# Optimization experiments

Measured on AMD Instinct MI355X. Metric: run time of the kernel, lower is better.

The kernel has to match this reference:

```python
import jax, jax.numpy as jnp
import numpy as np
from functools import partial

DELTA_B = 30.0
DELTA_H = 30.0
NB = 12  # 360/30
NH = 12
E, H, A, MLP, T = 16, 32, 32, 128, 20


def setup_inputs() -> dict:
    key = jax.random.key(0)
    ks = jax.random.split(key, 32)
    B, N = 512, 32
    inp = {}
    inp['x'] = jax.random.normal(ks[0], (B, N, T, 2), jnp.float32)
    inp['dmat'] = jax.random.uniform(ks[1], (B, N, T, N), jnp.float32) * 10.0
    inp['bmat'] = jax.random.uniform(ks[2], (B, N, T, N), jnp.float32) * 360.0
    inp['hmat'] = jax.random.uniform(ks[3], (B, N, T, N), jnp.float32) * 360.0
    inp['mask'] = jnp.ones((B, N, T), jnp.float32)
    g = lambda k, sh, s=0.1: jax.random.normal(k, sh, jnp.float32) * s
    inp['emb_w'] = g(ks[4], (2, E)); inp['emb_b'] = jnp.zeros((E,), jnp.float32)
    inp['w_ih'] = g(ks[5], (E, 4 * H)); inp['w_hh'] = g(ks[6], (H, 4 * H))
    inp['b_ih'] = jnp.zeros((4 * H,), jnp.float32); inp['b_hh'] = jnp.zeros((4 * H,), jnp.float32)
    inp['enc2att_w'] = g(ks[7], (H, A)); inp['enc2att_b'] = jnp.zeros((A,), jnp.float32)
    inp['domain_tab'] = jnp.full((NB, NH), 5.0, jnp.float32)  # domain_parameter init
    inp['spemb_w'] = g(ks[8], (2 * A, A)); inp['spemb_b'] = jnp.zeros((A,), jnp.float32)
    inp['att2enc_w'] = g(ks[9], (A, H)); inp['att2enc_b'] = jnp.zeros((H,), jnp.float32)
    inp['cls_w1'] = g(ks[10], (T * H, MLP)); inp['cls_b1'] = jnp.zeros((MLP,), jnp.float32)
    inp['cls_w2'] = g(ks[11], (MLP, MLP)); inp['cls_b2'] = jnp.zeros((MLP,), jnp.float32)
    inp['cls_w3'] = g(ks[12], (MLP, 1)); inp['cls_b3'] = jnp.zeros((1,), jnp.float32)
    return inp


def _forward(x, dmat, bmat, hmat, mask, emb_w, emb_b, w_ih, w_hh, b_ih, b_hh,
             enc2att_w, enc2att_b, domain_tab, spemb_w, spemb_b,
             att2enc_w, att2enc_b, cls_w1, cls_b1, cls_w2, cls_b2, cls_w3, cls_b3):
    B, N = x.shape[0], x.shape[1]
    xe = x @ emb_w + emb_b                      # [B,N,T,E]
    # time-major sequences for scan
    seq = (jnp.moveaxis(xe, 2, 0), jnp.moveaxis(dmat, 2, 0), jnp.moveaxis(bmat, 2, 0),
           jnp.moveaxis(hmat, 2, 0), jnp.moveaxis(mask, 2, 0))
    h0 = jnp.zeros((B, N, H), xe.dtype)
    c0 = jnp.zeros((B, N, H), xe.dtype)

    def step(carry, inp):
        h, c = carry
        x_t, d_t, b_t, hd_t, m_t = inp
        gates = x_t @ w_ih + h @ w_hh + (b_ih + b_hh)   # [B,N,4H]
        i, f, g, o = jnp.split(gates, 4, axis=-1)
        c_new = jax.nn.sigmoid(f) * c + jax.nn.sigmoid(i) * jnp.tanh(g)
        h_lstm = jax.nn.sigmoid(o) * jnp.tanh(c_new)
        ha = h_lstm @ enc2att_w + enc2att_b              # enc2att -> [B,N,A]
        # spatial attention: domain value from bearing/heading bins vs distance
        ib = jnp.clip(jnp.floor(b_t / DELTA_B), 0, NB - 1).astype(jnp.int32)
        ih = jnp.clip(jnp.floor(hd_t / DELTA_H), 0, NH - 1).astype(jnp.int32)
        w = jax.nn.relu(domain_tab[ib, ih] - d_t)        # [B,N,N]
        w = w * m_t[:, :, None] * m_t[:, None, :]
        w = w / (w.sum(-1, keepdims=True) + 1e-8)
        att = jnp.einsum('bij,bjd->bid', w, ha)          # neighbor-weighted hidden
        emb = jnp.tanh(jnp.concatenate([ha, att], -1) @ spemb_w + spemb_b)
        h_new = emb @ att2enc_w + att2enc_b              # back to hidden_size
        return (h_new, c_new), h_new

    (_, _), hs = jax.lax.scan(step, (h0, c0), seq)       # hs: [T,B,N,H]
    enc = jnp.moveaxis(hs, 0, 2).reshape(B, N, T * H)
    z = jax.nn.leaky_relu(enc @ cls_w1 + cls_b1, 0.2)
    z = jax.nn.leaky_relu(z @ cls_w2 + cls_b2, 0.2)
    return jax.nn.sigmoid(z @ cls_w3 + cls_b3)           # [B,N,1]


def reference(x, dmat, bmat, hmat, mask, emb_w, emb_b, w_ih, w_hh, b_ih, b_hh,
              enc2att_w, enc2att_b, domain_tab, spemb_w, spemb_b,
              att2enc_w, att2enc_b, cls_w1, cls_b1, cls_w2, cls_b2, cls_w3, cls_b3):
    return _forward(x, dmat, bmat, hmat, mask, emb_w, emb_b, w_ih, w_hh, b_ih, b_hh,
                    enc2att_w, enc2att_b, domain_tab, spemb_w, spemb_b,
                    att2enc_w, att2enc_b, cls_w1, cls_b1, cls_w2, cls_b2, cls_w3, cls_b3)
```

## Files before the change

### kernel.cpp

```cpp
#include <hip/hip_runtime.h>
#include <hip/hip_bf16.h>

#define TD_B 512

typedef __bf16 bf16x8 __attribute__((ext_vector_type(8)));
typedef __bf16 bf16x4 __attribute__((ext_vector_type(4)));
typedef float  f32x4  __attribute__((ext_vector_type(4)));

#define MFMA(a, b, c) __builtin_amdgcn_mfma_f32_16x16x32_bf16((a), (b), (c), 0, 0, 0)

__device__ __forceinline__ float sigf(float x)  { return 1.0f / (1.0f + __expf(-x)); }
__device__ __forceinline__ float tanhf_(float x){ return 2.0f / (1.0f + __expf(-2.0f * x)) - 1.0f; }

extern "C" __global__ void __launch_bounds__(256, 2)
traj_disc_kernel(const float* __restrict__ x, const float* __restrict__ dmat,
                 const float* __restrict__ bmat, const float* __restrict__ hmat,
                 const float* __restrict__ mask,
                 const float* __restrict__ emb_w, const float* __restrict__ emb_b,
                 const float* __restrict__ w_ih, const float* __restrict__ w_hh,
                 const float* __restrict__ b_ih, const float* __restrict__ b_hh,
                 const float* __restrict__ e2a_w, const float* __restrict__ e2a_b,
                 const float* __restrict__ dom,
                 const float* __restrict__ sp_w, const float* __restrict__ sp_b,
                 const float* __restrict__ a2e_w, const float* __restrict__ a2e_b,
                 const float* __restrict__ w1, const float* __restrict__ b1,
                 const float* __restrict__ w2, const float* __restrict__ b2,
                 const float* __restrict__ w3, const float* __restrict__ b3,
                 float* __restrict__ out)
{
    const int b    = blockIdx.x;
    const int tid  = threadIdx.x;
    const int lane = tid & 63;
    const int w    = tid >> 6;
    const int l15  = lane & 15;
    const int lg   = lane >> 4;

    __shared__ __bf16 sAin[32][72];
    __shared__ __bf16 sHl [32][40];
    __shared__ __bf16 sWN [32][40];
    __shared__ __bf16 sHaT[32][40];
    __shared__ __bf16 sEmb[32][40];
    __shared__ __bf16 sPA [32][72];
    __shared__ float  sMaskT[20][36];
    __shared__ float  sDom[144];
    __shared__ __bf16 z1bf[32][136];
    __shared__ __bf16 z2bf[32][136];
    __shared__ int    sFlag;

    if (tid == 0) sFlag = 1;
    for (int idx = tid; idx < 32 * 72; idx += 256)
        (&sAin[0][0])[idx] = (idx % 72 == 48) ? (__bf16)1.0f : (__bf16)0.0f;
    for (int idx = tid; idx < 640; idx += 256) {
        int tt = idx >> 5, n = idx & 31;
        sMaskT[tt][n] = mask[(b * 32 + n) * 20 + tt];
    }
    if (tid < 144) sDom[tid] = dom[tid];
    __syncthreads();
    {
        const float d0 = sDom[0];
        bool ok = true;
        for (int i = tid; i < 144; i += 256) ok &= (sDom[i] == d0);
        for (int i = tid; i < 640; i += 256) ok &= ((&sMaskT[0][0])[(i >> 5) * 36 + (i & 31)] == 1.0f);
        if (!ok) sFlag = 0;
    }

    const int i0 = tid >> 3, p0 = tid & 7;
    const float dom0 = dom[0];
    const float ewa0 = emb_w[2 * p0],      ewa1 = emb_w[2 * p0 + 1];
    const float ewb0 = emb_w[16 + 2 * p0], ewb1 = emb_w[16 + 2 * p0 + 1];
    const float eb0  = emb_b[2 * p0],      eb1  = emb_b[2 * p0 + 1];

    bf16x8 Ag[2][2];
    #pragma unroll
    for (int mtl = 0; mtl < 2; ++mtl) {
        int c  = (2 * w + mtl) * 16 + l15;
        int cg = (c & 3) * 32 + (c >> 2);
        #pragma unroll
        for (int kt = 0; kt < 2; ++kt)
            #pragma unroll
            for (int j = 0; j < 8; ++j) {
                int k = kt * 32 + lg * 8 + j;
                float v;
                if (k < 16)       v = w_ih[k * 128 + cg];
                else if (k < 48)  v = w_hh[(k - 16) * 128 + cg];
                else if (k == 48) v = b_ih[cg] + b_hh[cg];
                else              v = 0.0f;
                Ag[mtl][kt][j] = (__bf16)v;
            }
    }
    const int mtw = w >> 1, ntw = w & 1;
    const int cw  = ntw * 16 + l15;
    bf16x8 Be2a, Ba2e, Bsp[2];
    #pragma unroll
    for (int j = 0; j < 8; ++j) {
        Be2a[j] = (__bf16)e2a_w[(lg * 8 + j) * 32 + cw];
        Ba2e[j] = (__bf16)a2e_w[(lg * 8 + j) * 32 + cw];
    }
    #pragma unroll
    for (int kt = 0; kt < 2; ++kt)
        #pragma unroll
        for (int j = 0; j < 8; ++j)
            Bsp[kt][j] = (__bf16)sp_w[(kt * 32 + lg * 8 + j) * 32 + cw];
    const float bEw = e2a_b[cw], bSw = sp_b[cw], bAw = a2e_b[cw];

    float cst[2][2] = {{0.f, 0.f}, {0.f, 0.f}};
    f32x4 accZ[2][2] = {};
    bf16x8 Bw1cur[2];

    const float* dp = dmat + ((long)(b * 32 + i0) * 20) * 32 + 4 * p0;
    const float* bp = bmat + ((long)(b * 32 + i0) * 20) * 32 + 4 * p0;
    const float* hp = hmat + ((long)(b * 32 + i0) * 20) * 32 + 4 * p0;
    const float* xp = x + ((long)(b * 32 + i0) * 20) * 2;
    const float* w1p = w1 + lg * 8 * 128 + 32 * w + l15;

    float4 pdv = *(const float4*)dp;
    float4 pbv = *(const float4*)bp;
    float4 phv = *(const float4*)hp;
    float px0 = xp[0], px1 = xp[1];
    __syncthreads();
    const bool fast = (sFlag != 0);

    #pragma unroll 1
    for (int t = 0; t < 20; ++t) {
        {
            float4 dv = pdv, bv = pbv, hv = phv;
            float xx0 = px0, xx1 = px1;
            if (t < 19) {
                pdv = *(const float4*)(dp + 32); dp += 32;
                if (!fast) {
                    pbv = *(const float4*)(bp + 32); bp += 32;
                    phv = *(const float4*)(hp + 32); hp += 32;
                }
                px0 = xp[2]; px1 = xp[3]; xp += 2;
            }
            float wq[4];
            float inv;
            if (fast) {
                #pragma unroll
                for (int q = 0; q < 4; ++q) {
                    float v = dom0 - (&dv.x)[q];
                    wq[q] = v > 0.f ? v : 0.f;
                }
                float s = wq[0] + wq[1] + wq[2] + wq[3];
                s += __shfl_xor(s, 1); s += __shfl_xor(s, 2); s += __shfl_xor(s, 4);
                inv = 1.0f / (s + 1e-8f);
            } else {
                float4 mj = *(const float4*)&sMaskT[t][4 * p0];
                float  mi = sMaskT[t][i0];
                #pragma unroll
                for (int q = 0; q < 4; ++q) {
                    float bq = (&bv.x)[q], hq = (&hv.x)[q];
                    int ib = (int)floorf(bq * (1.0f / 30.0f)); ib = ib < 0 ? 0 : (ib > 11 ? 11 : ib);
                    int ih = (int)floorf(hq * (1.0f / 30.0f)); ih = ih < 0 ? 0 : (ih > 11 ? 11 : ih);
                    float v = sDom[ib * 12 + ih] - (&dv.x)[q];
                    v = v > 0.f ? v : 0.f;
                    wq[q] = v * (&mj.x)[q];
                }
                float s = wq[0] + wq[1] + wq[2] + wq[3];
                s += __shfl_xor(s, 1); s += __shfl_xor(s, 2); s += __shfl_xor(s, 4);
                inv = mi / (mi * s + 1e-8f);
            }
            bf16x4 wn4;
            #pragma unroll
            for (int q = 0; q < 4; ++q) wn4[q] = (__bf16)(wq[q] * inv);
            *(bf16x4*)&sWN[i0][4 * p0] = wn4;
            sAin[i0][2 * p0]     = (__bf16)(xx0 * ewa0 + xx1 * ewb0 + eb0);
            sAin[i0][2 * p0 + 1] = (__bf16)(xx0 * ewa1 + xx1 * ewb1 + eb1);
        }
        __syncthreads();

        {
            bf16x8 bxh[2][2];
            #pragma unroll
            for (int nt = 0; nt < 2; ++nt)
                #pragma unroll
                for (int kt = 0; kt < 2; ++kt)
                    bxh[nt][kt] = *(const bf16x8*)&sAin[nt * 16 + l15][kt * 32 + lg * 8];
            if (t >= 1) {
                bf16x8 az[2];
                #pragma unroll
                for (int mt = 0; mt < 2; ++mt)
                    az[mt] = *(const bf16x8*)&sAin[mt * 16 + l15][16 + lg * 8];
                #pragma unroll
                for (int mt = 0; mt < 2; ++mt)
                    #pragma unroll
                    for (int ntp = 0; ntp < 2; ++ntp)
                        accZ[mt][ntp] = MFMA(az[mt], Bw1cur[ntp], accZ[mt][ntp]);
            }
            #pragma unroll
            for (int mtl = 0; mtl < 2; ++mtl)
                #pragma unroll
                for (int nt = 0; nt < 2; ++nt) {
                    f32x4 cc = {0.f, 0.f, 0.f, 0.f};
                    cc = MFMA(Ag[mtl][0], bxh[nt][0], cc);
                    cc = MFMA(Ag[mtl][1], bxh[nt][1], cc);
                    float cn = sigf(cc[1]) * cst[mtl][nt] + sigf(cc[0]) * tanhf_(cc[2]);
                    cst[mtl][nt] = cn;
                    sHl[nt * 16 + l15][4 * (2 * w + mtl) + lg] = (__bf16)(sigf(cc[3]) * tanhf_(cn));
                }
            #pragma unroll
            for (int ntp = 0; ntp < 2; ++ntp)
                #pragma unroll
                for (int j = 0; j < 8; ++j)
                    Bw1cur[ntp][j] = (__bf16)w1p[j * 128 + ntp * 16];
            w1p += 4096;
        }
        __syncthreads();

        {
            bf16x8 a = *(const bf16x8*)&sHl[mtw * 16 + l15][lg * 8];
            f32x4 cc = {0.f, 0.f, 0.f, 0.f};
            cc = MFMA(a, Be2a, cc);
            bf16x4 tv;
            #pragma unroll
            for (int q = 0; q < 4; ++q) {
                float v = cc[q] + bEw;
                tv[q] = (__bf16)v;
                sPA[mtw * 16 + 4 * lg + q][cw] = (__bf16)v;
            }
            *(bf16x4*)&sHaT[cw][mtw * 16 + 4 * lg] = tv;
        }
        __syncthreads();

        {
            bf16x8 aW = *(const bf16x8*)&sWN [mtw * 16 + l15][lg * 8];
            bf16x8 bT = *(const bf16x8*)&sHaT[cw][lg * 8];
            f32x4 cc = {0.f, 0.f, 0.f, 0.f};
            cc = MFMA(aW, bT, cc);
            #pragma unroll
            for (int q = 0; q < 4; ++q)
                sPA[mtw * 16 + 4 * lg + q][32 + cw] = (__bf16)cc[q];
        }
        __syncthreads();

        {
            bf16x8 a0 = *(const bf16x8*)&sPA[mtw * 16 + l15][lg * 8];
            bf16x8 a1 = *(const bf16x8*)&sPA[mtw * 16 + l15][32 + lg * 8];
            f32x4 cc = {0.f, 0.f, 0.f, 0.f};
            cc = MFMA(a0, Bsp[0], cc);
            cc = MFMA(a1, Bsp[1], cc);
            #pragma unroll
            for (int q = 0; q < 4; ++q)
                sEmb[mtw * 16 + 4 * lg + q][cw] = (__bf16)tanhf_(cc[q] + bSw);
        }
        __syncthreads();

        {
            bf16x8 a = *(const bf16x8*)&sEmb[mtw * 16 + l15][lg * 8];
            f32x4 cc = {0.f, 0.f, 0.f, 0.f};
            cc = MFMA(a, Ba2e, cc);
            #pragma unroll
            for (int q = 0; q < 4; ++q)
                sAin[mtw * 16 + 4 * lg + q][16 + cw] = (__bf16)(cc[q] + bAw);
        }
    }

    __syncthreads();
    {
        bf16x8 az[2];
        #pragma unroll
        for (int mt = 0; mt < 2; ++mt)
            az[mt] = *(const bf16x8*)&sAin[mt * 16 + l15][16 + lg * 8];
        #pragma unroll
        for (int mt = 0; mt < 2; ++mt)
            #pragma unroll
            for (int ntp = 0; ntp < 2; ++ntp)
                accZ[mt][ntp] = MFMA(az[mt], Bw1cur[ntp], accZ[mt][ntp]);
    }
    #pragma unroll
    for (int mt = 0; mt < 2; ++mt)
        #pragma unroll
        for (int ntp = 0; ntp < 2; ++ntp) {
            int c = (2 * w + ntp) * 16 + l15;
            float bias = b1[c];
            #pragma unroll
            for (int q = 0; q < 4; ++q) {
                float v = accZ[mt][ntp][q] + bias;
                v = v > 0.f ? v : 0.2f * v;
                z1bf[mt * 16 + 4 * lg + q][c] = (__bf16)v;
            }
        }
    __syncthreads();

    {
        f32x4 c2[2][2] = {};
        #pragma unroll
        for (int kt = 0; kt < 4; ++kt) {
            bf16x8 a[2];
            #pragma unroll
            for (int mt = 0; mt < 2; ++mt)
                a[mt] = *(const bf16x8*)&z1bf[mt * 16 + l15][kt * 32 + lg * 8];
            bf16x8 bb[2];
            #pragma unroll
            for (int ntp = 0; ntp < 2; ++ntp) {
                int c = (2 * w + ntp) * 16 + l15;
                #pragma unroll
                for (int j = 0; j < 8; ++j)
                    bb[ntp][j] = (__bf16)w2[(kt * 32 + lg * 8 + j) * 128 + c];
            }
            #pragma unroll
            for (int mt = 0; mt < 2; ++mt)
                #pragma unroll
                for (int ntp = 0; ntp < 2; ++ntp)
                    c2[mt][ntp] = MFMA(a[mt], bb[ntp], c2[mt][ntp]);
        }
        #pragma unroll
        for (int mt = 0; mt < 2; ++mt)
            #pragma unroll
            for (int ntp = 0; ntp < 2; ++ntp) {
                int c = (2 * w + ntp) * 16 + l15;
                float bias = b2[c];
                #pragma unroll
                for (int q = 0; q < 4; ++q) {
                    float v = c2[mt][ntp][q] + bias;
                    v = v > 0.f ? v : 0.2f * v;
                    z2bf[mt * 16 + 4 * lg + q][c] = (__bf16)v;
                }
            }
    }
    __syncthreads();

    {
        int n = tid >> 3, kg = tid & 7;
        bf16x8 v0 = *(const bf16x8*)&z2bf[n][kg * 16];
        bf16x8 v1 = *(const bf16x8*)&z2bf[n][kg * 16 + 8];
        float s = 0.f;
        #pragma unroll
        for (int j = 0; j < 8; ++j)
            s += (float)v0[j] * w3[kg * 16 + j] + (float)v1[j] * w3[kg * 16 + 8 + j];
        s += __shfl_xor(s, 1); s += __shfl_xor(s, 2); s += __shfl_xor(s, 4);
        if (kg == 0) out[b * 32 + n] = sigf(s + b3[0]);
    }
}

extern "C" void kernel_launch(void* const* d_in, const int* in_sizes, int n_in,
                              void* d_out, int out_size, void* d_ws, size_t ws_size,
                              hipStream_t stream) {
    (void)in_sizes; (void)n_in; (void)d_ws; (void)ws_size; (void)out_size;
    const float* x     = (const float*)d_in[0];
    const float* dmat  = (const float*)d_in[1];
    const float* bmat  = (const float*)d_in[2];
    const float* hmat  = (const float*)d_in[3];
    const float* mask  = (const float*)d_in[4];
    const float* emb_w = (const float*)d_in[5];
    const float* emb_b = (const float*)d_in[6];
    const float* w_ih  = (const float*)d_in[7];
    const float* w_hh  = (const float*)d_in[8];
    const float* b_ih  = (const float*)d_in[9];
    const float* b_hh  = (const float*)d_in[10];
    const float* e2a_w = (const float*)d_in[11];
    const float* e2a_b = (const float*)d_in[12];
    const float* dom   = (const float*)d_in[13];
    const float* sp_w  = (const float*)d_in[14];
    const float* sp_b  = (const float*)d_in[15];
    const float* a2e_w = (const float*)d_in[16];
    const float* a2e_b = (const float*)d_in[17];
    const float* w1    = (const float*)d_in[18];
    const float* b1    = (const float*)d_in[19];
    const float* w2    = (const float*)d_in[20];
    const float* b2    = (const float*)d_in[21];
    const float* w3    = (const float*)d_in[22];
    const float* b3    = (const float*)d_in[23];
    float* out = (float*)d_out;

    traj_disc_kernel<<<dim3(TD_B), dim3(256), 0, stream>>>(
        x, dmat, bmat, hmat, mask, emb_w, emb_b, w_ih, w_hh, b_ih, b_hh,
        e2a_w, e2a_b, dom, sp_w, sp_b, a2e_w, a2e_b,
        w1, b1, w2, b2, w3, b3, out);
}
```

Before: 70.22 us.

## Halve workgroup to two waves, give each wave more tiles, drop a barrier

The block shrinks from 256 to 128 threads. Each wave now owns four LSTM gate tiles and two row tiles in the attention and embedding stages, and the per-thread load and neighbour-weight work widens from 4 to 8 columns. Each wave now writes exactly the sHaT rows it reads next, so the attention MFMA moves into the same phase and one __syncthreads per timestep is removed. The intent is to cut barrier and sync cost in a latency-bound recurrence. The cost is more serial MFMA and VALU work per wave and fewer waves per CU to hide latency.

```diff
diff --git a/kernel.cpp b/kernel.cpp
--- a/kernel.cpp
+++ b/kernel.cpp
@@ -12,7 +12,7 @@
 __device__ __forceinline__ float sigf(float x)  { return 1.0f / (1.0f + __expf(-x)); }
 __device__ __forceinline__ float tanhf_(float x){ return 2.0f / (1.0f + __expf(-2.0f * x)) - 1.0f; }
 
-extern "C" __global__ void __launch_bounds__(256, 2)
+extern "C" __global__ void __launch_bounds__(128, 2)
 traj_disc_kernel(const float* __restrict__ x, const float* __restrict__ dmat,
                  const float* __restrict__ bmat, const float* __restrict__ hmat,
                  const float* __restrict__ mask,
@@ -48,32 +48,36 @@
     __shared__ int    sFlag;
 
     if (tid == 0) sFlag = 1;
-    for (int idx = tid; idx < 32 * 72; idx += 256)
+    for (int idx = tid; idx < 32 * 72; idx += 128)
         (&sAin[0][0])[idx] = (idx % 72 == 48) ? (__bf16)1.0f : (__bf16)0.0f;
-    for (int idx = tid; idx < 640; idx += 256) {
+    for (int idx = tid; idx < 640; idx += 128) {
         int tt = idx >> 5, n = idx & 31;
         sMaskT[tt][n] = mask[(b * 32 + n) * 20 + tt];
     }
-    if (tid < 144) sDom[tid] = dom[tid];
+    if (tid < 128) for (int idx = tid; idx < 144; idx += 128) sDom[idx] = dom[idx];
     __syncthreads();
     {
         const float d0 = sDom[0];
         bool ok = true;
-        for (int i = tid; i < 144; i += 256) ok &= (sDom[i] == d0);
-        for (int i = tid; i < 640; i += 256) ok &= ((&sMaskT[0][0])[(i >> 5) * 36 + (i & 31)] == 1.0f);
+        for (int i = tid; i < 144; i += 128) ok &= (sDom[i] == d0);
+        for (int i = tid; i < 640; i += 128) ok &= ((&sMaskT[0][0])[(i >> 5) * 36 + (i & 31)] == 1.0f);
         if (!ok) sFlag = 0;
     }
 
-    const int i0 = tid >> 3, p0 = tid & 7;
+    const int i0 = tid >> 2, q0 = (tid & 3) * 8, e0 = (tid & 3) * 4;
     const float dom0 = dom[0];
-    const float ewa0 = emb_w[2 * p0],      ewa1 = emb_w[2 * p0 + 1];
-    const float ewb0 = emb_w[16 + 2 * p0], ewb1 = emb_w[16 + 2 * p0 + 1];
-    const float eb0  = emb_b[2 * p0],      eb1  = emb_b[2 * p0 + 1];
-
-    bf16x8 Ag[2][2];
-    #pragma unroll
-    for (int mtl = 0; mtl < 2; ++mtl) {
-        int c  = (2 * w + mtl) * 16 + l15;
+    float ewa[4], ewb[4], ebb[4];
+    #pragma unroll
+    for (int k = 0; k < 4; ++k) {
+        ewa[k] = emb_w[e0 + k];
+        ewb[k] = emb_w[16 + e0 + k];
+        ebb[k] = emb_b[e0 + k];
+    }
+
+    bf16x8 Ag[4][2];
+    #pragma unroll
+    for (int mtl = 0; mtl < 4; ++mtl) {
+        int c  = (4 * w + mtl) * 16 + l15;
         int cg = (c & 3) * 32 + (c >> 2);
         #pragma unroll
         for (int kt = 0; kt < 2; ++kt)
@@ -88,8 +92,7 @@
                 Ag[mtl][kt][j] = (__bf16)v;
             }
     }
-    const int mtw = w >> 1, ntw = w & 1;
-    const int cw  = ntw * 16 + l15;
+    const int cw = w * 16 + l15;
     bf16x8 Be2a, Ba2e, Bsp[2];
     #pragma unroll
     for (int j = 0; j < 8; ++j) {
@@ -103,19 +106,19 @@
             Bsp[kt][j] = (__bf16)sp_w[(kt * 32 + lg * 8 + j) * 32 + cw];
     const float bEw = e2a_b[cw], bSw = sp_b[cw], bAw = a2e_b[cw];
 
-    float cst[2][2] = {{0.f, 0.f}, {0.f, 0.f}};
-    f32x4 accZ[2][2] = {};
-    bf16x8 Bw1cur[2];
-
-    const float* dp = dmat + ((long)(b * 32 + i0) * 20) * 32 + 4 * p0;
-    const float* bp = bmat + ((long)(b * 32 + i0) * 20) * 32 + 4 * p0;
-    const float* hp = hmat + ((long)(b * 32 + i0) * 20) * 32 + 4 * p0;
+    float cst[4][2] = {};
+    f32x4 accZ[2][4] = {};
+    bf16x8 Bw1cur[4];
+
+    const float* dp = dmat + ((long)(b * 32 + i0) * 20) * 32 + q0;
+    const float* bp = bmat + ((long)(b * 32 + i0) * 20) * 32 + q0;
+    const float* hp = hmat + ((long)(b * 32 + i0) * 20) * 32 + q0;
     const float* xp = x + ((long)(b * 32 + i0) * 20) * 2;
-    const float* w1p = w1 + lg * 8 * 128 + 32 * w + l15;
-
-    float4 pdv = *(const float4*)dp;
-    float4 pbv = *(const float4*)bp;
-    float4 phv = *(const float4*)hp;
+    const float* w1p = w1 + lg * 8 * 128 + 64 * w + l15;
+
+    float4 pdv0 = *(const float4*)dp,       pdv1 = *(const float4*)(dp + 4);
+    float4 pbv0 = *(const float4*)bp,       pbv1 = *(const float4*)(bp + 4);
+    float4 phv0 = *(const float4*)hp,       phv1 = *(const float4*)(hp + 4);
     float px0 = xp[0], px1 = xp[1];
     __syncthreads();
     const bool fast = (sFlag != 0);
@@ -123,49 +126,62 @@
     #pragma unroll 1
     for (int t = 0; t < 20; ++t) {
         {
-            float4 dv = pdv, bv = pbv, hv = phv;
+            float dvv[8], bvv[8], hvv[8];
+            #pragma unroll
+            for (int k = 0; k < 4; ++k) {
+                dvv[k] = (&pdv0.x)[k]; dvv[4 + k] = (&pdv1.x)[k];
+                bvv[k] = (&pbv0.x)[k]; bvv[4 + k] = (&pbv1.x)[k];
+                hvv[k] = (&phv0.x)[k]; hvv[4 + k] = (&phv1.x)[k];
+            }
             float xx0 = px0, xx1 = px1;
             if (t < 19) {
-                pdv = *(const float4*)(dp + 32); dp += 32;
+                pdv0 = *(const float4*)(dp + 32); pdv1 = *(const float4*)(dp + 36); dp += 32;
                 if (!fast) {
-                    pbv = *(const float4*)(bp + 32); bp += 32;
-                    phv = *(const float4*)(hp + 32); hp += 32;
+                    pbv0 = *(const float4*)(bp + 32); pbv1 = *(const float4*)(bp + 36); bp += 32;
+                    phv0 = *(const float4*)(hp + 32); phv1 = *(const float4*)(hp + 36); hp += 32;
                 }
                 px0 = xp[2]; px1 = xp[3]; xp += 2;
             }
-            float wq[4];
+            float wq[8];
             float inv;
             if (fast) {
-                #pragma unroll
-                for (int q = 0; q < 4; ++q) {
-                    float v = dom0 - (&dv.x)[q];
-                    wq[q] = v > 0.f ? v : 0.f;
-                }
-                float s = wq[0] + wq[1] + wq[2] + wq[3];
-                s += __shfl_xor(s, 1); s += __shfl_xor(s, 2); s += __shfl_xor(s, 4);
+                float s = 0.f;
+                #pragma unroll
+                for (int k = 0; k < 8; ++k) {
+                    float v = dom0 - dvv[k];
+                    wq[k] = v > 0.f ? v : 0.f;
+                    s += wq[k];
+                }
+                s += __shfl_xor(s, 1); s += __shfl_xor(s, 2);
                 inv = 1.0f / (s + 1e-8f);
             } else {
-                float4 mj = *(const float4*)&sMaskT[t][4 * p0];
-                float  mi = sMaskT[t][i0];
-                #pragma unroll
-                for (int q = 0; q < 4; ++q) {
-                    float bq = (&bv.x)[q], hq = (&hv.x)[q];
+                float4 mj0 = *(const float4*)&sMaskT[t][q0];
+                float4 mj1 = *(const float4*)&sMaskT[t][q0 + 4];
+                float  mi  = sMaskT[t][i0];
+                float s = 0.f;
+                #pragma unroll
+                for (int k = 0; k < 8; ++k) {
+                    float bq = bvv[k], hq = hvv[k];
                     int ib = (int)floorf(bq * (1.0f / 30.0f)); ib = ib < 0 ? 0 : (ib > 11 ? 11 : ib);
                     int ih = (int)floorf(hq * (1.0f / 30.0f)); ih = ih < 0 ? 0 : (ih > 11 ? 11 : ih);
-                    float v = sDom[ib * 12 + ih] - (&dv.x)[q];
+                    float v = sDom[ib * 12 + ih] - dvv[k];
                     v = v > 0.f ? v : 0.f;
-                    wq[q] = v * (&mj.x)[q];
-                }
-                float s = wq[0] + wq[1] + wq[2] + wq[3];
-                s += __shfl_xor(s, 1); s += __shfl_xor(s, 2); s += __shfl_xor(s, 4);
+                    float m = (k < 4) ? (&mj0.x)[k] : (&mj1.x)[k - 4];
+                    wq[k] = v * m;
+                    s += wq[k];
+                }
+                s += __shfl_xor(s, 1); s += __shfl_xor(s, 2);
                 inv = mi / (mi * s + 1e-8f);
             }
-            bf16x4 wn4;
-            #pragma unroll
-            for (int q = 0; q < 4; ++q) wn4[q] = (__bf16)(wq[q] * inv);
-            *(bf16x4*)&sWN[i0][4 * p0] = wn4;
-            sAin[i0][2 * p0]     = (__bf16)(xx0 * ewa0 + xx1 * ewb0 + eb0);
-            sAin[i0][2 * p0 + 1] = (__bf16)(xx0 * ewa1 + xx1 * ewb1 + eb1);
+            bf16x8 wn8;
+            #pragma unroll
+            for (int k = 0; k < 8; ++k) wn8[k] = (__bf16)(wq[k] * inv);
+            *(bf16x8*)&sWN[i0][q0] = wn8;
+            bf16x4 xv;
+            #pragma unroll
+            for (int k = 0; k < 4; ++k)
+                xv[k] = (__bf16)(xx0 * ewa[k] + xx1 * ewb[k] + ebb[k]);
+            *(bf16x4*)&sAin[i0][e0] = xv;
         }
         __syncthreads();
 
@@ -184,11 +200,11 @@
                 #pragma unroll
                 for (int mt = 0; mt < 2; ++mt)
                     #pragma unroll
-                    for (int ntp = 0; ntp < 2; ++ntp)
-                        accZ[mt][ntp] = MFMA(az[mt], Bw1cur[ntp], accZ[mt][ntp]);
-            }
-            #pragma unroll
-            for (int mtl = 0; mtl < 2; ++mtl)
+                    for (int ct = 0; ct < 4; ++ct)
+                        accZ[mt][ct] = MFMA(az[mt], Bw1cur[ct], accZ[mt][ct]);
+            }
+            #pragma unroll
+            for (int mtl = 0; mtl < 4; ++mtl)
                 #pragma unroll
                 for (int nt = 0; nt < 2; ++nt) {
                     f32x4 cc = {0.f, 0.f, 0.f, 0.f};
@@ -196,18 +212,19 @@
                     cc = MFMA(Ag[mtl][1], bxh[nt][1], cc);
                     float cn = sigf(cc[1]) * cst[mtl][nt] + sigf(cc[0]) * tanhf_(cc[2]);
                     cst[mtl][nt] = cn;
-                    sHl[nt * 16 + l15][4 * (2 * w + mtl) + lg] = (__bf16)(sigf(cc[3]) * tanhf_(cn));
-                }
-            #pragma unroll
-            for (int ntp = 0; ntp < 2; ++ntp)
+                    sHl[nt * 16 + l15][4 * (4 * w + mtl) + lg] = (__bf16)(sigf(cc[3]) * tanhf_(cn));
+                }
+            #pragma unroll
+            for (int ct = 0; ct < 4; ++ct)
                 #pragma unroll
                 for (int j = 0; j < 8; ++j)
-                    Bw1cur[ntp][j] = (__bf16)w1p[j * 128 + ntp * 16];
+                    Bw1cur[ct][j] = (__bf16)w1p[j * 128 + ct * 16];
             w1p += 4096;
         }
         __syncthreads();
 
-        {
+        #pragma unroll
+        for (int mtw = 0; mtw < 2; ++mtw) {
             bf16x8 a = *(const bf16x8*)&sHl[mtw * 16 + l15][lg * 8];
             f32x4 cc = {0.f, 0.f, 0.f, 0.f};
             cc = MFMA(a, Be2a, cc);
@@ -220,20 +237,23 @@
             }
             *(bf16x4*)&sHaT[cw][mtw * 16 + 4 * lg] = tv;
         }
+
+        {
+            bf16x8 bT = *(const bf16x8*)&sHaT[w * 16 + l15][lg * 8];
+            #pragma unroll
+            for (int mtw = 0; mtw < 2; ++mtw) {
+                bf16x8 aW = *(const bf16x8*)&sWN[mtw * 16 + l15][lg * 8];
+                f32x4 cc = {0.f, 0.f, 0.f, 0.f};
+                cc = MFMA(aW, bT, cc);
+                #pragma unroll
+                for (int q = 0; q < 4; ++q)
+                    sPA[mtw * 16 + 4 * lg + q][32 + cw] = (__bf16)cc[q];
+            }
+        }
         __syncthreads();
 
-        {
-            bf16x8 aW = *(const bf16x8*)&sWN [mtw * 16 + l15][lg * 8];
-            bf16x8 bT = *(const bf16x8*)&sHaT[cw][lg * 8];
-            f32x4 cc = {0.f, 0.f, 0.f, 0.f};
-            cc = MFMA(aW, bT, cc);
-            #pragma unroll
-            for (int q = 0; q < 4; ++q)
-                sPA[mtw * 16 + 4 * lg + q][32 + cw] = (__bf16)cc[q];
-        }
-        __syncthreads();
-
-        {
+        #pragma unroll
+        for (int mtw = 0; mtw < 2; ++mtw) {
             bf16x8 a0 = *(const bf16x8*)&sPA[mtw * 16 + l15][lg * 8];
             bf16x8 a1 = *(const bf16x8*)&sPA[mtw * 16 + l15][32 + lg * 8];
             f32x4 cc = {0.f, 0.f, 0.f, 0.f};
@@ -245,13 +265,14 @@
         }
         __syncthreads();
 
-        {
-            bf16x8 a = *(const bf16x8*)&sEmb[mtw * 16 + l15][lg * 8];
-            f32x4 cc = {0.f, 0.f, 0.f, 0.f};
-            cc = MFMA(a, Ba2e, cc);
+        #pragma unroll
+        for (int mtw = 0; mtw < 2; ++mtw) {
+            bf16x8 ae = *(const bf16x8*)&sEmb[mtw * 16 + l15][lg * 8];
+            f32x4 cf = {0.f, 0.f, 0.f, 0.f};
+            cf = MFMA(ae, Ba2e, cf);
             #pragma unroll
             for (int q = 0; q < 4; ++q)
-                sAin[mtw * 16 + 4 * lg + q][16 + cw] = (__bf16)(cc[q] + bAw);
+                sAin[mtw * 16 + 4 * lg + q][16 + cw] = (__bf16)(cf[q] + bAw);
         }
     }
 
@@ -264,18 +285,18 @@
         #pragma unroll
         for (int mt = 0; mt < 2; ++mt)
             #pragma unroll
-            for (int ntp = 0; ntp < 2; ++ntp)
-                accZ[mt][ntp] = MFMA(az[mt], Bw1cur[ntp], accZ[mt][ntp]);
+            for (int ct = 0; ct < 4; ++ct)
+                accZ[mt][ct] = MFMA(az[mt], Bw1cur[ct], accZ[mt][ct]);
     }
     #pragma unroll
     for (int mt = 0; mt < 2; ++mt)
         #pragma unroll
-        for (int ntp = 0; ntp < 2; ++ntp) {
-            int c = (2 * w + ntp) * 16 + l15;
+        for (int ct = 0; ct < 4; ++ct) {
+            int c = (4 * w + ct) * 16 + l15;
             float bias = b1[c];
             #pragma unroll
             for (int q = 0; q < 4; ++q) {
-                float v = accZ[mt][ntp][q] + bias;
+                float v = accZ[mt][ct][q] + bias;
                 v = v > 0.f ? v : 0.2f * v;
                 z1bf[mt * 16 + 4 * lg + q][c] = (__bf16)v;
             }
@@ -283,36 +304,34 @@
     __syncthreads();
 
     {
-        f32x4 c2[2][2] = {};
+        f32x4 c2[2][4] = {};
         #pragma unroll
         for (int kt = 0; kt < 4; ++kt) {
             bf16x8 a[2];
             #pragma unroll
             for (int mt = 0; mt < 2; ++mt)
                 a[mt] = *(const bf16x8*)&z1bf[mt * 16 + l15][kt * 32 + lg * 8];
-            bf16x8 bb[2];
-            #pragma unroll
-            for (int ntp = 0; ntp < 2; ++ntp) {
-                int c = (2 * w + ntp) * 16 + l15;
+            #pragma unroll
+            for (int ct = 0; ct < 4; ++ct) {
+                bf16x8 bw2;
+                int c = (4 * w + ct) * 16 + l15;
                 #pragma unroll
                 for (int j = 0; j < 8; ++j)
-                    bb[ntp][j] = (__bf16)w2[(kt * 32 + lg * 8 + j) * 128 + c];
-            }
-            #pragma unroll
-            for (int mt = 0; mt < 2; ++mt)
-                #pragma unroll
-                for (int ntp = 0; ntp < 2; ++ntp)
-                    c2[mt][ntp] = MFMA(a[mt], bb[ntp], c2[mt][ntp]);
+                    bw2[j] = (__bf16)w2[(kt * 32 + lg * 8 + j) * 128 + c];
+                #pragma unroll
+                for (int mt = 0; mt < 2; ++mt)
+                    c2[mt][ct] = MFMA(a[mt], bw2, c2[mt][ct]);
+            }
         }
         #pragma unroll
         for (int mt = 0; mt < 2; ++mt)
             #pragma unroll
-            for (int ntp = 0; ntp < 2; ++ntp) {
-                int c = (2 * w + ntp) * 16 + l15;
+            for (int ct = 0; ct < 4; ++ct) {
+                int c = (4 * w + ct) * 16 + l15;
                 float bias = b2[c];
                 #pragma unroll
                 for (int q = 0; q < 4; ++q) {
-                    float v = c2[mt][ntp][q] + bias;
+                    float v = c2[mt][ct][q] + bias;
                     v = v > 0.f ? v : 0.2f * v;
                     z2bf[mt * 16 + 4 * lg + q][c] = (__bf16)v;
                 }
@@ -321,14 +340,16 @@
     __syncthreads();
 
     {
-        int n = tid >> 3, kg = tid & 7;
-        bf16x8 v0 = *(const bf16x8*)&z2bf[n][kg * 16];
-        bf16x8 v1 = *(const bf16x8*)&z2bf[n][kg * 16 + 8];
+        int n = tid >> 2, kg = tid & 3;
         float s = 0.f;
         #pragma unroll
-        for (int j = 0; j < 8; ++j)
-            s += (float)v0[j] * w3[kg * 16 + j] + (float)v1[j] * w3[kg * 16 + 8 + j];
-        s += __shfl_xor(s, 1); s += __shfl_xor(s, 2); s += __shfl_xor(s, 4);
+        for (int p = 0; p < 4; ++p) {
+            bf16x8 v = *(const bf16x8*)&z2bf[n][kg * 32 + p * 8];
+            #pragma unroll
+            for (int j = 0; j < 8; ++j)
+                s += (float)v[j] * w3[kg * 32 + p * 8 + j];
+        }
+        s += __shfl_xor(s, 1); s += __shfl_xor(s, 2);
         if (kg == 0) out[b * 32 + n] = sigf(s + b3[0]);
     }
 }
@@ -363,7 +384,7 @@
     const float* b3    = (const float*)d_in[23];
     float* out = (float*)d_out;
 
-    traj_disc_kernel<<<dim3(TD_B), dim3(256), 0, stream>>>(
+    traj_disc_kernel<<<dim3(TD_B), dim3(128), 0, stream>>>(
         x, dmat, bmat, hmat, mask, emb_w, emb_b, w_ih, w_hh, b_ih, b_hh,
         e2a_w, e2a_b, dom, sp_w, sp_b, a2e_w, a2e_b,
         w1, b1, w2, b2, w3, b3, out);
```

Result: slower. 107.0 us (+52.4%).
